# Kernel optimization log

Measured on AMD Instinct MI355X. Metric: run time of the kernel, lower is better.

## Reference

```python
import math
import jax, jax.numpy as jnp
import numpy as np

SCALE = 64.0
MARGIN = 0.5
COS_M = math.cos(MARGIN)
SIN_M = math.sin(MARGIN)
TH = math.cos(math.pi - MARGIN)
MM = math.sin(math.pi - MARGIN) * MARGIN
EPS = 1e-12  # F.normalize default eps

B, D, C = 2048, 512, 100000


def setup_inputs() -> dict:
    key = jax.random.key(0)
    k1, k2, k3 = jax.random.split(key, 3)
    embeddings = jax.random.normal(k1, (B, D), dtype=jnp.float32)
    labels = jax.random.randint(k2, (B,), 0, C, dtype=jnp.int64)
    # xavier-uniform-like init for weight [C, D]
    limit = math.sqrt(6.0 / (C + D))
    weight = jax.random.uniform(k3, (C, D), dtype=jnp.float32, minval=-limit, maxval=limit)
    return {"embeddings": embeddings, "labels": labels, "weight": weight}


def _l2norm(x):
    n = jnp.linalg.norm(x, axis=-1, keepdims=True)
    return x / jnp.maximum(n, EPS)


def reference(embeddings, labels, weight):
    cosine = _l2norm(embeddings) @ _l2norm(weight).T  # [B, C]
    sine = jnp.sqrt(jnp.clip(1.0 - cosine * cosine, 0.0, None))
    phi = cosine * COS_M - sine * SIN_M
    phi = jnp.where(cosine > TH, phi, cosine - MM)
    # one-hot blend without materializing a separate one-hot tensor
    col = jnp.arange(cosine.shape[1])[None, :]
    is_target = col == labels[:, None]  # [B, C] bool
    logits = jnp.where(is_target, phi, cosine)
    return logits * SCALE
```

## Files before the change

kernel.cpp:

```cpp
#include <hip/hip_runtime.h>
#include <hip/hip_bf16.h>
#include <math.h>

constexpr int Bq = 2048;
constexpr int Dq = 512;
constexpr int Cq = 100000;
constexpr int NPAD = 100096;

constexpr float SCALE = 64.0f;
constexpr float COS_M = 0.8775825618903728f;
constexpr float SIN_M = 0.479425538604203f;
constexpr float THR   = -0.8775825618903728f;
constexpr float MM    = 0.2397127693021015f;

typedef __attribute__((ext_vector_type(8))) __bf16 bf16x8;
typedef __attribute__((ext_vector_type(4))) float f32x4;

typedef const __attribute__((address_space(1))) unsigned int guint;
typedef __attribute__((address_space(3))) unsigned int suint;

__device__ __forceinline__ void gload_lds16(const unsigned short* g, unsigned short* lds)
{
    __builtin_amdgcn_global_load_lds((guint*)g, (suint*)lds, 16, 0, 0);
}

__device__ __forceinline__ unsigned int pack_bf16x2(float lo, float hi)
{
    __hip_bfloat16 h0 = __float2bfloat16(lo);
    __hip_bfloat16 h1 = __float2bfloat16(hi);
    return ((unsigned int)(*(unsigned short*)&h1) << 16) |
           (unsigned int)(*(unsigned short*)&h0);
}

__global__ __launch_bounds__(256) void normalize_rows_kernel(
    const float* __restrict__ in, unsigned short* __restrict__ out, int nrows)
{
    const int w = threadIdx.x >> 6, lane = threadIdx.x & 63;
    const int row = blockIdx.x * 4 + w;
    float4 a = {0.f, 0.f, 0.f, 0.f}, b = a;
    if (row < nrows) {
        const float4* src = reinterpret_cast<const float4*>(in + (size_t)row * Dq);
        a = src[lane];
        b = src[lane + 64];
    }
    float ss = a.x * a.x + a.y * a.y + a.z * a.z + a.w * a.w
             + b.x * b.x + b.y * b.y + b.z * b.z + b.w * b.w;
    #pragma unroll
    for (int off = 32; off > 0; off >>= 1) ss += __shfl_down(ss, off);
    ss = __shfl(ss, 0);
    const float invn = 1.0f / fmaxf(sqrtf(ss), 1e-12f);

    uint2* out64 = reinterpret_cast<uint2*>(out + (size_t)row * Dq);
    uint2 pa, pb;
    pa.x = pack_bf16x2(a.x * invn, a.y * invn);
    pa.y = pack_bf16x2(a.z * invn, a.w * invn);
    pb.x = pack_bf16x2(b.x * invn, b.y * invn);
    pb.y = pack_bf16x2(b.z * invn, b.w * invn);
    out64[lane] = pa;
    out64[lane + 64] = pb;
}

__global__ __launch_bounds__(256, 4) void arc_gemm_kernel(
    const unsigned short* __restrict__ A,
    const unsigned short* __restrict__ Bn,
    const int* __restrict__ labels,
    float* __restrict__ out)
{
    extern __shared__ unsigned short lds[];

    const int cpx = (int)gridDim.x >> 3;
    const int bid = ((int)blockIdx.x & 7) * cpx + ((int)blockIdx.x >> 3);
    const int tm = bid & 15;
    const int tn = bid >> 4;
    const int m0 = tm * 128, n0 = tn * 128;

    const int t = threadIdx.x;
    const int w = t >> 6, lane = t & 63;
    const int wr = (w >> 1) * 64;
    const int wc = (w & 1) * 64;
    const int fr = lane & 15, kg = lane >> 4;
    const int cfrag = (kg ^ ((fr >> 1) & 3)) * 8;

    const int trow = t >> 2;
    const int sch = ((t & 3) ^ ((trow >> 1) & 3)) * 8;
    const unsigned short* gA = A  + (size_t)(m0 + trow) * Dq + sch;
    const unsigned short* gB = Bn + (size_t)(n0 + trow) * Dq + sch;
    const int dst = t * 8;

#define STAGE_A(buf, u, kts) gload_lds16(gA + (size_t)(u) * 64 * Dq + (kts) * 32, \
                                         &lds[(buf) * 8192 + (u) * 2048 + dst])
#define STAGE_B(buf, u, kts) gload_lds16(gB + (size_t)(u) * 64 * Dq + (kts) * 32, \
                                         &lds[(buf) * 8192 + 4096 + (u) * 2048 + dst])
#define BARRIER() do { __builtin_amdgcn_sched_barrier(0); __builtin_amdgcn_s_barrier(); } while (0)

    f32x4 acc[4][4];
    #pragma unroll
    for (int i = 0; i < 4; ++i)
        #pragma unroll
        for (int j = 0; j < 4; ++j) acc[i][j] = {0.f, 0.f, 0.f, 0.f};

    STAGE_A(0, 0, 0); STAGE_A(0, 1, 0); STAGE_B(0, 0, 0); STAGE_B(0, 1, 0);
    STAGE_A(1, 0, 1); STAGE_A(1, 1, 1); STAGE_B(1, 0, 1); STAGE_B(1, 1, 1);
    asm volatile("s_waitcnt vmcnt(4)" ::: "memory");
    __builtin_amdgcn_s_barrier();

    const int arow = (wr + fr) * 32 + cfrag;
    const int brow = 4096 + (wc + fr) * 32 + cfrag;

    #pragma unroll
    for (int kt = 0; kt < 16; ++kt) {
        const int cb = kt & 1;
        const int cbo = cb * 8192;
        bf16x8 afr[4], bfr[4];
        #pragma unroll
        for (int mi = 0; mi < 4; ++mi)
            afr[mi] = *reinterpret_cast<const bf16x8*>(&lds[cbo + arow + mi * 512]);
        #pragma unroll
        for (int ni = 0; ni < 4; ++ni)
            bfr[ni] = *reinterpret_cast<const bf16x8*>(&lds[cbo + brow + ni * 512]);
        asm volatile("s_waitcnt lgkmcnt(0)" ::: "memory");
        BARRIER();
        if (kt < 14) {
            STAGE_A(cb, 0, kt + 2); STAGE_A(cb, 1, kt + 2);
            STAGE_B(cb, 0, kt + 2); STAGE_B(cb, 1, kt + 2);
        }
        __builtin_amdgcn_s_setprio(1);
        #pragma unroll
        for (int mi = 0; mi < 4; ++mi)
            #pragma unroll
            for (int ni = 0; ni < 4; ++ni)
                acc[mi][ni] = __builtin_amdgcn_mfma_f32_16x16x32_bf16(
                    bfr[ni], afr[mi], acc[mi][ni], 0, 0, 0);
        __builtin_amdgcn_s_setprio(0);
        if (kt < 14) asm volatile("s_waitcnt vmcnt(4)" ::: "memory");
        else         asm volatile("s_waitcnt vmcnt(0)" ::: "memory");
        BARRIER();
    }

    float* lf = reinterpret_cast<float*>(lds);
    #pragma unroll
    for (int pass = 0; pass < 2; ++pass) {
        if ((w >> 1) == pass) {
            #pragma unroll
            for (int mi = 0; mi < 4; ++mi) {
                const int lrow = mi * 16 + fr;
                const int lab = labels[m0 + pass * 64 + lrow];
                #pragma unroll
                for (int ni = 0; ni < 4; ++ni) {
                    const int col0 = wc + ni * 16 + kg * 4;
                    const int gcol0 = n0 + col0;
                    f32x4 v = acc[mi][ni];
                    #pragma unroll
                    for (int r = 0; r < 4; ++r) {
                        if (gcol0 + r == lab) {
                            float c = v[r];
                            float sine = sqrtf(fmaxf(1.0f - c * c, 0.0f));
                            float phi = c * COS_M - sine * SIN_M;
                            v[r] = (c > THR) ? phi : (c - MM);
                        }
                    }
                    v *= SCALE;
                    *reinterpret_cast<f32x4*>(&lf[lrow * 132 + col0]) = v;
                }
            }
        }
        __syncthreads();
        const int cc = t & 31, rh = t >> 5;
        #pragma unroll
        for (int s = 0; s < 8; ++s) {
            const int lrow = s * 8 + rh;
            f32x4 v = *reinterpret_cast<const f32x4*>(&lf[lrow * 132 + cc * 4]);
            const int gcol0 = n0 + cc * 4;
            if (gcol0 < Cq)
                __builtin_nontemporal_store(
                    v, reinterpret_cast<f32x4*>(
                        out + (size_t)(m0 + pass * 64 + lrow) * Cq + gcol0));
        }
        __syncthreads();
    }
#undef STAGE_A
#undef STAGE_B
#undef BARRIER
}

extern "C" void kernel_launch(void* const* d_in, const int* in_sizes, int n_in,
                              void* d_out, int out_size, void* d_ws, size_t ws_size,
                              hipStream_t stream)
{
    const float* emb    = (const float*)d_in[0];
    const int*   labels = (const int*)d_in[1];
    const float* weight = (const float*)d_in[2];
    float* out = (float*)d_out;

    unsigned short* Abf = (unsigned short*)d_ws;
    unsigned short* Bbf = Abf + (size_t)Bq * Dq;

    normalize_rows_kernel<<<Bq / 4, 256, 0, stream>>>(emb, Abf, Bq);
    normalize_rows_kernel<<<NPAD / 4, 256, 0, stream>>>(weight, Bbf, Cq);
    arc_gemm_kernel<<<16 * (NPAD / 128), 256, 33792, stream>>>(Abf, Bbf, labels, out);
}
```

Before: 335.8 us.

## Load B fragments directly to registers and double K-tile depth

The GEMM now stages only the A tile through LDS, using 64-wide K tiles with an 8-way XOR swizzle. Each wave loads its own B fragments straight from global memory into double-buffered registers, prefetching one K step ahead. This removes half the LDS traffic and halves the number of K iterations and barriers. In exchange it raises register pressure (occupancy hint drops from 4 to 2 waves per SIMD), and the direct B loads are less coalesced, 16-byte per-lane reads.

```diff
diff --git a/kernel.cpp b/kernel.cpp
--- a/kernel.cpp
+++ b/kernel.cpp
@@ -60,7 +60,7 @@
     out64[lane + 64] = pb;
 }
 
-__global__ __launch_bounds__(256, 4) void arc_gemm_kernel(
+__global__ __launch_bounds__(256, 2) void arc_gemm_kernel(
     const unsigned short* __restrict__ A,
     const unsigned short* __restrict__ Bn,
     const int* __restrict__ labels,
@@ -79,61 +79,79 @@
     const int wr = (w >> 1) * 64;
     const int wc = (w & 1) * 64;
     const int fr = lane & 15, kg = lane >> 4;
-    const int cfrag = (kg ^ ((fr >> 1) & 3)) * 8;
-
-    const int trow = t >> 2;
-    const int sch = ((t & 3) ^ ((trow >> 1) & 3)) * 8;
-    const unsigned short* gA = A  + (size_t)(m0 + trow) * Dq + sch;
-    const unsigned short* gB = Bn + (size_t)(n0 + trow) * Dq + sch;
-    const int dst = t * 8;
-
-#define STAGE_A(buf, u, kts) gload_lds16(gA + (size_t)(u) * 64 * Dq + (kts) * 32, \
-                                         &lds[(buf) * 8192 + (u) * 2048 + dst])
-#define STAGE_B(buf, u, kts) gload_lds16(gB + (size_t)(u) * 64 * Dq + (kts) * 32, \
-                                         &lds[(buf) * 8192 + 4096 + (u) * 2048 + dst])
+    const int s7 = fr & 7;
+    const int c0 = (kg ^ s7) * 8;
+    const int c1 = ((4 + kg) ^ s7) * 8;
+
+    const int trow = t >> 3;
+    const int tch = ((t & 7) ^ (trow & 7)) * 8;
+    const unsigned short* gA = A + (size_t)(m0 + trow) * Dq + tch;
+    const int dstA = trow * 64 + (t & 7) * 8;
+
+#define STAGE_A(buf, s, kts) gload_lds16(gA + (size_t)(s) * 32 * Dq + (size_t)(kts) * 64, \
+                                         &lds[(buf) * 8192 + (s) * 2048 + dstA])
 #define BARRIER() do { __builtin_amdgcn_sched_barrier(0); __builtin_amdgcn_s_barrier(); } while (0)
 
+    const unsigned short* bp0 = Bn + (size_t)(n0 + wc + fr) * Dq + kg * 8;
+
     f32x4 acc[4][4];
     #pragma unroll
     for (int i = 0; i < 4; ++i)
         #pragma unroll
         for (int j = 0; j < 4; ++j) acc[i][j] = {0.f, 0.f, 0.f, 0.f};
 
-    STAGE_A(0, 0, 0); STAGE_A(0, 1, 0); STAGE_B(0, 0, 0); STAGE_B(0, 1, 0);
-    STAGE_A(1, 0, 1); STAGE_A(1, 1, 1); STAGE_B(1, 0, 1); STAGE_B(1, 1, 1);
-    asm volatile("s_waitcnt vmcnt(4)" ::: "memory");
+    bf16x8 bA[4][2], bB[4][2];
+
+    STAGE_A(0, 0, 0); STAGE_A(0, 1, 0); STAGE_A(0, 2, 0); STAGE_A(0, 3, 0);
+    STAGE_A(1, 0, 1); STAGE_A(1, 1, 1); STAGE_A(1, 2, 1); STAGE_A(1, 3, 1);
+    #pragma unroll
+    for (int ni = 0; ni < 4; ++ni)
+        #pragma unroll
+        for (int ks = 0; ks < 2; ++ks)
+            bA[ni][ks] = *reinterpret_cast<const bf16x8*>(
+                bp0 + (size_t)ni * 16 * Dq + ks * 32);
+    asm volatile("s_waitcnt vmcnt(12)" ::: "memory");
     __builtin_amdgcn_s_barrier();
 
-    const int arow = (wr + fr) * 32 + cfrag;
-    const int brow = 4096 + (wc + fr) * 32 + cfrag;
-
-    #pragma unroll
-    for (int kt = 0; kt < 16; ++kt) {
-        const int cb = kt & 1;
-        const int cbo = cb * 8192;
-        bf16x8 afr[4], bfr[4];
-        #pragma unroll
-        for (int mi = 0; mi < 4; ++mi)
-            afr[mi] = *reinterpret_cast<const bf16x8*>(&lds[cbo + arow + mi * 512]);
-        #pragma unroll
-        for (int ni = 0; ni < 4; ++ni)
-            bfr[ni] = *reinterpret_cast<const bf16x8*>(&lds[cbo + brow + ni * 512]);
+    const int arow = (wr + fr) * 64;
+
+    #pragma unroll
+    for (int kt = 0; kt < 8; ++kt) {
+        const int cbo = (kt & 1) * 8192;
+        bf16x8 (&bcur)[4][2] = (kt & 1) ? bB : bA;
+        bf16x8 (&bnxt)[4][2] = (kt & 1) ? bA : bB;
+        bf16x8 afr[4][2];
+        #pragma unroll
+        for (int mi = 0; mi < 4; ++mi) {
+            afr[mi][0] = *reinterpret_cast<const bf16x8*>(&lds[cbo + arow + mi * 1024 + c0]);
+            afr[mi][1] = *reinterpret_cast<const bf16x8*>(&lds[cbo + arow + mi * 1024 + c1]);
+        }
         asm volatile("s_waitcnt lgkmcnt(0)" ::: "memory");
         BARRIER();
-        if (kt < 14) {
-            STAGE_A(cb, 0, kt + 2); STAGE_A(cb, 1, kt + 2);
-            STAGE_B(cb, 0, kt + 2); STAGE_B(cb, 1, kt + 2);
+        if (kt < 6) {
+            STAGE_A(kt & 1, 0, kt + 2); STAGE_A(kt & 1, 1, kt + 2);
+            STAGE_A(kt & 1, 2, kt + 2); STAGE_A(kt & 1, 3, kt + 2);
+        }
+        if (kt < 7) {
+            #pragma unroll
+            for (int ni = 0; ni < 4; ++ni)
+                #pragma unroll
+                for (int ks = 0; ks < 2; ++ks)
+                    bnxt[ni][ks] = *reinterpret_cast<const bf16x8*>(
+                        bp0 + (size_t)ni * 16 * Dq + (kt + 1) * 64 + ks * 32);
         }
         __builtin_amdgcn_s_setprio(1);
         #pragma unroll
         for (int mi = 0; mi < 4; ++mi)
             #pragma unroll
             for (int ni = 0; ni < 4; ++ni)
-                acc[mi][ni] = __builtin_amdgcn_mfma_f32_16x16x32_bf16(
-                    bfr[ni], afr[mi], acc[mi][ni], 0, 0, 0);
+                #pragma unroll
+                for (int ks = 0; ks < 2; ++ks)
+                    acc[mi][ni] = __builtin_amdgcn_mfma_f32_16x16x32_bf16(
+                        bcur[ni][ks], afr[mi][ks], acc[mi][ni], 0, 0, 0);
         __builtin_amdgcn_s_setprio(0);
-        if (kt < 14) asm volatile("s_waitcnt vmcnt(4)" ::: "memory");
-        else         asm volatile("s_waitcnt vmcnt(0)" ::: "memory");
+        if (kt < 6)       asm volatile("s_waitcnt vmcnt(12)" ::: "memory");
+        else if (kt == 6) asm volatile("s_waitcnt vmcnt(8)"  ::: "memory");
         BARRIER();
     }
 
@@ -179,7 +197,6 @@
         __syncthreads();
     }
 #undef STAGE_A
-#undef STAGE_B
 #undef BARRIER
 }
 
```

Result: slower. 584.9 us (+74.2%).
